# Kernel tuning notes

Measured on AMD Instinct MI355X. Metric: run time of the kernel, lower is better.

## Reference

```python
import jax, jax.numpy as jnp
import numpy as np

NUM_EMBEDDINGS = 1024
EMBEDDING_DIM = 64
COMMITMENT_COST = 0.25


def setup_inputs() -> dict:
    key = jax.random.key(0)
    k1, k2 = jax.random.split(key)
    inputs = jax.random.normal(k1, (16, 4096, EMBEDDING_DIM), dtype=jnp.float32)
    # codebook initialized uniform(-1/K, 1/K) as in the torch module
    emb_weight = jax.random.uniform(
        k2, (NUM_EMBEDDINGS, EMBEDDING_DIM), dtype=jnp.float32,
        minval=-1.0 / NUM_EMBEDDINGS, maxval=1.0 / NUM_EMBEDDINGS)
    return {"inputs": inputs, "emb_weight": emb_weight}


def reference(inputs, emb_weight):
    B, T, D = inputs.shape
    flat = inputs.reshape(-1, D)  # [N, D]
    distances = (jnp.sum(flat * flat, axis=1, keepdims=True)
                 + jnp.sum(emb_weight * emb_weight, axis=1)
                 - 2.0 * jnp.matmul(flat, emb_weight.T))
    encoding_indices = jnp.argmin(distances, axis=1)  # [N]
    # one-hot @ codebook == direct gather
    quantized = emb_weight[encoding_indices]  # [N, D]
    q_latent_loss = jnp.mean((jax.lax.stop_gradient(quantized) - flat) ** 2)
    e_latent_loss = jnp.mean((quantized - jax.lax.stop_gradient(flat)) ** 2)
    loss = q_latent_loss + COMMITMENT_COST * e_latent_loss
    # straight-through estimator
    quantized_st = flat + jax.lax.stop_gradient(quantized - flat)
    quantized_st = quantized_st.reshape(B, T, D)
    return quantized_st, loss, encoding_indices[:, None]
```

## Files before the change

### kernel.cpp

```cpp
#include <hip/hip_runtime.h>

typedef float f4 __attribute__((ext_vector_type(4)));
typedef __attribute__((ext_vector_type(4))) float f32x4;
typedef __attribute__((ext_vector_type(8))) short bf16x8;

#define NV 65536
#define D 64
#define K 1024
#define BM 64
#define MARGIN 4.0e-3f
#define CAP 32
#define LOSS_OFF 4194304
#define IDX_OFF  4194305

__device__ __forceinline__ unsigned f2bf(float f) {
  unsigned u = __builtin_bit_cast(unsigned, f);
  return (u + 0x7fffu + ((u >> 16) & 1u)) >> 16;
}

__global__ void vq_prep(const float* __restrict__ E, float* __restrict__ ws,
                        float* __restrict__ loss) {
  const int n = blockIdx.x * 256 + threadIdx.x;
  unsigned short* Ebf = reinterpret_cast<unsigned short*>(ws + K);
  if (n == 0) *loss = 0.0f;
  if (n < K) {
    const float* row = E + (size_t)n * D;
    float r[8];
#pragma unroll
    for (int j = 0; j < 8; ++j) r[j] = __fmul_rn(row[j], row[j]);
#pragma unroll
    for (int i = 8; i < D; i += 8)
#pragma unroll
      for (int j = 0; j < 8; ++j)
        r[j] = __fadd_rn(r[j], __fmul_rn(row[i + j], row[i + j]));
    ws[n] = __fadd_rn(
        __fadd_rn(__fadd_rn(r[0], r[1]), __fadd_rn(r[2], r[3])),
        __fadd_rn(__fadd_rn(r[4], r[5]), __fadd_rn(r[6], r[7])));
  }
  const int fi = n >> 6, lane = n & 63;
  const int ct = fi >> 1, half = fi & 1;
  const int code = ct * 16 + (lane & 15);
  const int d0 = half * 32 + (lane >> 4) * 8;
  const float* src = E + (size_t)code * D + d0;
  f4 a = *reinterpret_cast<const f4*>(src);
  f4 b = *reinterpret_cast<const f4*>(src + 4);
  uint4 pk;
  pk.x = f2bf(a[0]) | (f2bf(a[1]) << 16);
  pk.y = f2bf(a[2]) | (f2bf(a[3]) << 16);
  pk.z = f2bf(b[0]) | (f2bf(b[1]) << 16);
  pk.w = f2bf(b[2]) | (f2bf(b[3]) << 16);
  *reinterpret_cast<uint4*>(Ebf + (size_t)n * 8) = pk;
}

__device__ __forceinline__ bf16x8 ld_a(const float* p) {
  f4 a = *reinterpret_cast<const f4*>(p);
  f4 b = *reinterpret_cast<const f4*>(p + 4);
  bf16x8 r;
  r[0] = (short)f2bf(a[0]); r[1] = (short)f2bf(a[1]);
  r[2] = (short)f2bf(a[2]); r[3] = (short)f2bf(a[3]);
  r[4] = (short)f2bf(b[0]); r[5] = (short)f2bf(b[1]);
  r[6] = (short)f2bf(b[2]); r[7] = (short)f2bf(b[3]);
  return r;
}

__global__ __launch_bounds__(256, 2) void vq_main(
    const float* __restrict__ X, const float* __restrict__ E,
    const float* __restrict__ ws, float* __restrict__ out) {
  __shared__ float eSqL[K];
  __shared__ unsigned cntL[BM];
  __shared__ unsigned short candL[BM * CAP];
  __shared__ int sidxL[BM];

  const unsigned short* Ebf = reinterpret_cast<const unsigned short*>(ws + K);

  const int t = threadIdx.x;
  const int lane = t & 63;
  const int w = t >> 6;
  const int l15 = lane & 15, l4 = lane >> 4;
  const int bv0 = blockIdx.x * BM;

  const float* xv = X + (size_t)(bv0 + w * 16 + l15) * D;
  bf16x8 a0 = ld_a(xv + l4 * 8);
  bf16x8 a1 = ld_a(xv + 32 + l4 * 8);

#pragma unroll
  for (int i = 0; i < 4; ++i) eSqL[t + 256 * i] = ws[t + 256 * i];
  if (t < BM) cntL[t] = 0;
  __syncthreads();

  const unsigned short* ebase = Ebf + (size_t)lane * 8;

  float umin[4];
#pragma unroll
  for (int r = 0; r < 4; ++r) umin[r] = 3.4e38f;
#pragma unroll 4
  for (int ct = 0; ct < 64; ++ct) {
    bf16x8 b0 = *reinterpret_cast<const bf16x8*>(ebase + ct * 1024);
    bf16x8 b1 = *reinterpret_cast<const bf16x8*>(ebase + ct * 1024 + 512);
    f32x4 acc = {0.f, 0.f, 0.f, 0.f};
    acc = __builtin_amdgcn_mfma_f32_16x16x32_bf16(a0, b0, acc, 0, 0, 0);
    acc = __builtin_amdgcn_mfma_f32_16x16x32_bf16(a1, b1, acc, 0, 0, 0);
    const float ee = eSqL[ct * 16 + l15];
#pragma unroll
    for (int r = 0; r < 4; ++r)
      umin[r] = fminf(umin[r], __fmaf_rn(-2.0f, acc[r], ee));
  }
  float thr[4];
#pragma unroll
  for (int r = 0; r < 4; ++r) {
#pragma unroll
    for (int off = 1; off < 16; off <<= 1)
      umin[r] = fminf(umin[r], __shfl_xor(umin[r], off, 64));
    thr[r] = umin[r] + MARGIN;
  }

#pragma unroll 4
  for (int ct = 0; ct < 64; ++ct) {
    bf16x8 b0 = *reinterpret_cast<const bf16x8*>(ebase + ct * 1024);
    bf16x8 b1 = *reinterpret_cast<const bf16x8*>(ebase + ct * 1024 + 512);
    f32x4 acc = {0.f, 0.f, 0.f, 0.f};
    acc = __builtin_amdgcn_mfma_f32_16x16x32_bf16(a0, b0, acc, 0, 0, 0);
    acc = __builtin_amdgcn_mfma_f32_16x16x32_bf16(a1, b1, acc, 0, 0, 0);
    const int gc = ct * 16 + l15;
    const float ee = eSqL[gc];
#pragma unroll
    for (int r = 0; r < 4; ++r) {
      if (__fmaf_rn(-2.0f, acc[r], ee) <= thr[r]) {
        const int v = w * 16 + l4 * 4 + r;
        const unsigned pos = atomicAdd(&cntL[v], 1u);
        if (pos < CAP) candL[v * CAP + pos] = (unsigned short)gc;
      }
    }
  }
  __syncthreads();

  {
    const int v = t >> 2, par = t & 3;
    const int gv = bv0 + v;
    const float* xr = X + (size_t)gv * D;
    float rr[8];
#pragma unroll
    for (int j = 0; j < 8; ++j) rr[j] = __fmul_rn(xr[j], xr[j]);
#pragma unroll
    for (int i = 8; i < 64; i += 8)
#pragma unroll
      for (int j = 0; j < 8; ++j)
        rr[j] = __fadd_rn(rr[j], __fmul_rn(xr[i + j], xr[i + j]));
    const float xx = __fadd_rn(
        __fadd_rn(__fadd_rn(rr[0], rr[1]), __fadd_rn(rr[2], rr[3])),
        __fadd_rn(__fadd_rn(rr[4], rr[5]), __fadd_rn(rr[6], rr[7])));

    float best = 3.4e38f;
    int bi = 0x7fffffff;
    const unsigned n = cntL[v];
    if (n <= CAP) {
      for (unsigned i = par; i < n; i += 4) {
        const int c = candL[v * CAP + i];
        const float* er = E + (size_t)c * D;
        float m = 0.f;
#pragma unroll
        for (int j = 0; j < 64; ++j) m = fmaf(er[j], xr[j], m);
        const float dd = __fsub_rn(__fadd_rn(xx, eSqL[c]), 2.0f * m);
        if (dd < best || (dd == best && c < bi)) { best = dd; bi = c; }
      }
    } else {
      for (int c = par; c < K; c += 4) {
        const float* er = E + (size_t)c * D;
        float m = 0.f;
#pragma unroll
        for (int j = 0; j < 64; ++j) m = fmaf(er[j], xr[j], m);
        const float dd = __fsub_rn(__fadd_rn(xx, eSqL[c]), 2.0f * m);
        if (dd < best || (dd == best && c < bi)) { best = dd; bi = c; }
      }
    }
#pragma unroll
    for (int off = 1; off < 4; off <<= 1) {
      const float ov = __shfl_xor(best, off, 64);
      const int oi = __shfl_xor(bi, off, 64);
      if (ov < best || (ov == best && oi < bi)) { best = ov; bi = oi; }
    }
    if (par == 0) sidxL[v] = bi;
  }
  __syncthreads();

  {
    const int v = t >> 2, h = t & 3;
    const int gv = bv0 + v;
    const int code = sidxL[v];
    const f4* er = reinterpret_cast<const f4*>(E + (size_t)code * D + h * 16);
    const f4* xr = reinterpret_cast<const f4*>(X + (size_t)gv * D + h * 16);
    f4* op = reinterpret_cast<f4*>(out + (size_t)gv * D + h * 16);
    float lsum = 0.f;
#pragma unroll
    for (int i = 0; i < 4; ++i) {
      f4 e4 = er[i], x4 = xr[i];
      float d0 = e4[0] - x4[0], d1 = e4[1] - x4[1];
      float d2 = e4[2] - x4[2], d3 = e4[3] - x4[3];
      lsum += d0 * d0 + d1 * d1 + d2 * d2 + d3 * d3;
      op[i] = e4;
    }
    if (t < BM) out[IDX_OFF + bv0 + t] = (float)sidxL[t];
#pragma unroll
    for (int off = 1; off < 64; off <<= 1) lsum += __shfl_xor(lsum, off, 64);
    if (lane == 0)
      atomicAdd(out + LOSS_OFF, lsum * (1.25f / (float)(NV * (size_t)D)));
  }
}

extern "C" void kernel_launch(void* const* d_in, const int* in_sizes, int n_in,
                              void* d_out, int out_size, void* d_ws, size_t ws_size,
                              hipStream_t stream) {
  const float* X = (const float*)d_in[0];
  const float* E = (const float*)d_in[1];
  float* out = (float*)d_out;
  float* ws = (float*)d_ws;
  vq_prep<<<32, 256, 0, stream>>>(E, ws, out + LOSS_OFF);
  vq_main<<<NV / BM, 256, 0, stream>>>(X, E, ws, out);
}
```

Measured before the change: 105.8 us.

## Process 128 rows per block with two MFMA row tiles per wave

Doubles the rows handled per block, so each wave computes two 16-row MFMA tiles that share the same codebook fragment loads. This halves the number of bf16 codebook reads per row. The rescore and output phases now use 2 threads per row instead of 4. The block count halves, which reduces parallelism in the scalar rescore phase and increases register pressure.

```diff
diff --git a/kernel.cpp b/kernel.cpp
--- a/kernel.cpp
+++ b/kernel.cpp
@@ -7,7 +7,8 @@
 #define NV 65536
 #define D 64
 #define K 1024
-#define BM 64
+#define NT 256
+#define BM 128
 #define MARGIN 4.0e-3f
 #define CAP 32
 #define LOSS_OFF 4194304
@@ -63,7 +64,7 @@
   return r;
 }
 
-__global__ __launch_bounds__(256, 2) void vq_main(
+__global__ __launch_bounds__(NT, 2) void vq_main(
     const float* __restrict__ X, const float* __restrict__ E,
     const float* __restrict__ ws, float* __restrict__ out) {
   __shared__ float eSqL[K];
@@ -79,63 +80,77 @@
   const int l15 = lane & 15, l4 = lane >> 4;
   const int bv0 = blockIdx.x * BM;
 
-  const float* xv = X + (size_t)(bv0 + w * 16 + l15) * D;
-  bf16x8 a0 = ld_a(xv + l4 * 8);
-  bf16x8 a1 = ld_a(xv + 32 + l4 * 8);
-
-#pragma unroll
-  for (int i = 0; i < 4; ++i) eSqL[t + 256 * i] = ws[t + 256 * i];
+  const float* xv0 = X + (size_t)(bv0 + w * 32 + l15) * D;
+  const float* xv1 = xv0 + 16 * D;
+  bf16x8 a00 = ld_a(xv0 + l4 * 8);
+  bf16x8 a01 = ld_a(xv0 + 32 + l4 * 8);
+  bf16x8 a10 = ld_a(xv1 + l4 * 8);
+  bf16x8 a11 = ld_a(xv1 + 32 + l4 * 8);
+
+#pragma unroll
+  for (int i = 0; i < 4; ++i) eSqL[t + NT * i] = ws[t + NT * i];
   if (t < BM) cntL[t] = 0;
   __syncthreads();
 
   const unsigned short* ebase = Ebf + (size_t)lane * 8;
 
-  float umin[4];
-#pragma unroll
-  for (int r = 0; r < 4; ++r) umin[r] = 3.4e38f;
-#pragma unroll 4
+  float umin[8];
+#pragma unroll
+  for (int r = 0; r < 8; ++r) umin[r] = 3.4e38f;
+#pragma unroll 8
   for (int ct = 0; ct < 64; ++ct) {
     bf16x8 b0 = *reinterpret_cast<const bf16x8*>(ebase + ct * 1024);
     bf16x8 b1 = *reinterpret_cast<const bf16x8*>(ebase + ct * 1024 + 512);
-    f32x4 acc = {0.f, 0.f, 0.f, 0.f};
-    acc = __builtin_amdgcn_mfma_f32_16x16x32_bf16(a0, b0, acc, 0, 0, 0);
-    acc = __builtin_amdgcn_mfma_f32_16x16x32_bf16(a1, b1, acc, 0, 0, 0);
+    f32x4 acc0 = {0.f, 0.f, 0.f, 0.f}, acc1 = {0.f, 0.f, 0.f, 0.f};
+    acc0 = __builtin_amdgcn_mfma_f32_16x16x32_bf16(a00, b0, acc0, 0, 0, 0);
+    acc0 = __builtin_amdgcn_mfma_f32_16x16x32_bf16(a01, b1, acc0, 0, 0, 0);
+    acc1 = __builtin_amdgcn_mfma_f32_16x16x32_bf16(a10, b0, acc1, 0, 0, 0);
+    acc1 = __builtin_amdgcn_mfma_f32_16x16x32_bf16(a11, b1, acc1, 0, 0, 0);
     const float ee = eSqL[ct * 16 + l15];
 #pragma unroll
-    for (int r = 0; r < 4; ++r)
-      umin[r] = fminf(umin[r], __fmaf_rn(-2.0f, acc[r], ee));
-  }
-  float thr[4];
-#pragma unroll
-  for (int r = 0; r < 4; ++r) {
+    for (int r = 0; r < 4; ++r) {
+      umin[r]     = fminf(umin[r],     __fmaf_rn(-2.0f, acc0[r], ee));
+      umin[4 + r] = fminf(umin[4 + r], __fmaf_rn(-2.0f, acc1[r], ee));
+    }
+  }
+  float thr[8];
+#pragma unroll
+  for (int r = 0; r < 8; ++r) {
 #pragma unroll
     for (int off = 1; off < 16; off <<= 1)
       umin[r] = fminf(umin[r], __shfl_xor(umin[r], off, 64));
     thr[r] = umin[r] + MARGIN;
   }
 
-#pragma unroll 4
+#pragma unroll 8
   for (int ct = 0; ct < 64; ++ct) {
     bf16x8 b0 = *reinterpret_cast<const bf16x8*>(ebase + ct * 1024);
     bf16x8 b1 = *reinterpret_cast<const bf16x8*>(ebase + ct * 1024 + 512);
-    f32x4 acc = {0.f, 0.f, 0.f, 0.f};
-    acc = __builtin_amdgcn_mfma_f32_16x16x32_bf16(a0, b0, acc, 0, 0, 0);
-    acc = __builtin_amdgcn_mfma_f32_16x16x32_bf16(a1, b1, acc, 0, 0, 0);
+    f32x4 acc0 = {0.f, 0.f, 0.f, 0.f}, acc1 = {0.f, 0.f, 0.f, 0.f};
+    acc0 = __builtin_amdgcn_mfma_f32_16x16x32_bf16(a00, b0, acc0, 0, 0, 0);
+    acc0 = __builtin_amdgcn_mfma_f32_16x16x32_bf16(a01, b1, acc0, 0, 0, 0);
+    acc1 = __builtin_amdgcn_mfma_f32_16x16x32_bf16(a10, b0, acc1, 0, 0, 0);
+    acc1 = __builtin_amdgcn_mfma_f32_16x16x32_bf16(a11, b1, acc1, 0, 0, 0);
     const int gc = ct * 16 + l15;
     const float ee = eSqL[gc];
 #pragma unroll
     for (int r = 0; r < 4; ++r) {
-      if (__fmaf_rn(-2.0f, acc[r], ee) <= thr[r]) {
-        const int v = w * 16 + l4 * 4 + r;
+      if (__fmaf_rn(-2.0f, acc0[r], ee) <= thr[r]) {
+        const int v = w * 32 + l4 * 4 + r;
         const unsigned pos = atomicAdd(&cntL[v], 1u);
         if (pos < CAP) candL[v * CAP + pos] = (unsigned short)gc;
       }
+      if (__fmaf_rn(-2.0f, acc1[r], ee) <= thr[4 + r]) {
+        const int v = w * 32 + 16 + l4 * 4 + r;
+        const unsigned pos = atomicAdd(&cntL[v], 1u);
+        if (pos < CAP) candL[v * CAP + pos] = (unsigned short)gc;
+      }
     }
   }
   __syncthreads();
 
   {
-    const int v = t >> 2, par = t & 3;
+    const int v = t >> 1, par = t & 1;
     const int gv = bv0 + v;
     const float* xr = X + (size_t)gv * D;
     float rr[8];
@@ -154,7 +169,7 @@
     int bi = 0x7fffffff;
     const unsigned n = cntL[v];
     if (n <= CAP) {
-      for (unsigned i = par; i < n; i += 4) {
+      for (unsigned i = par; i < n; i += 2) {
         const int c = candL[v * CAP + i];
         const float* er = E + (size_t)c * D;
         float m = 0.f;
@@ -164,7 +179,7 @@
         if (dd < best || (dd == best && c < bi)) { best = dd; bi = c; }
       }
     } else {
-      for (int c = par; c < K; c += 4) {
+      for (int c = par; c < K; c += 2) {
         const float* er = E + (size_t)c * D;
         float m = 0.f;
 #pragma unroll
@@ -173,26 +188,23 @@
         if (dd < best || (dd == best && c < bi)) { best = dd; bi = c; }
       }
     }
-#pragma unroll
-    for (int off = 1; off < 4; off <<= 1) {
-      const float ov = __shfl_xor(best, off, 64);
-      const int oi = __shfl_xor(bi, off, 64);
-      if (ov < best || (ov == best && oi < bi)) { best = ov; bi = oi; }
-    }
+    const float ov = __shfl_xor(best, 1, 64);
+    const int oi = __shfl_xor(bi, 1, 64);
+    if (ov < best || (ov == best && oi < bi)) { best = ov; bi = oi; }
     if (par == 0) sidxL[v] = bi;
   }
   __syncthreads();
 
   {
-    const int v = t >> 2, h = t & 3;
+    const int v = t >> 1, h = t & 1;
     const int gv = bv0 + v;
     const int code = sidxL[v];
-    const f4* er = reinterpret_cast<const f4*>(E + (size_t)code * D + h * 16);
-    const f4* xr = reinterpret_cast<const f4*>(X + (size_t)gv * D + h * 16);
-    f4* op = reinterpret_cast<f4*>(out + (size_t)gv * D + h * 16);
+    const f4* er = reinterpret_cast<const f4*>(E + (size_t)code * D + h * 32);
+    const f4* xr = reinterpret_cast<const f4*>(X + (size_t)gv * D + h * 32);
+    f4* op = reinterpret_cast<f4*>(out + (size_t)gv * D + h * 32);
     float lsum = 0.f;
 #pragma unroll
-    for (int i = 0; i < 4; ++i) {
+    for (int i = 0; i < 8; ++i) {
       f4 e4 = er[i], x4 = xr[i];
       float d0 = e4[0] - x4[0], d1 = e4[1] - x4[1];
       float d2 = e4[2] - x4[2], d3 = e4[3] - x4[3];
@@ -215,5 +227,5 @@
   float* out = (float*)d_out;
   float* ws = (float*)d_ws;
   vq_prep<<<32, 256, 0, stream>>>(E, ws, out + LOSS_OFF);
-  vq_main<<<NV / BM, 256, 0, stream>>>(X, E, ws, out);
-}
+  vq_main<<<NV / BM, NT, 0, stream>>>(X, E, ws, out);
+}
```

New measurement: 98.45 us. 7.0% less time.
